# Kernel tuning notes

Measured on AMD Instinct MI355X. Metric: run time of the kernel, lower is better.

The kernel has to match this reference:

```python
import jax, jax.numpy as jnp
import numpy as np

B, IN, H, L, OUT, T, S0 = 512, 64, 512, 2, 12, 31, 8
HEAD = (T - 1) / 2  # 15.0
EPS = 1e-5


def setup_inputs() -> dict:
    key = jax.random.key(0)
    ks = jax.random.split(key, 10)
    s = 0.05
    return {
        "Wih0": jax.random.normal(ks[0], (4 * H, IN), jnp.float32) * s,
        "Whh0": jax.random.normal(ks[1], (4 * H, H), jnp.float32) * s,
        "b0": jax.random.normal(ks[2], (4 * H,), jnp.float32) * s,
        "Wih1": jax.random.normal(ks[3], (4 * H, H), jnp.float32) * s,
        "Whh1": jax.random.normal(ks[4], (4 * H, H), jnp.float32) * s,
        "b1": jax.random.normal(ks[5], (4 * H,), jnp.float32) * s,
        "gamma": jnp.ones((H,), jnp.float32),
        "beta": jnp.zeros((H,), jnp.float32),
        "Wout": jax.random.normal(ks[6], (OUT, H), jnp.float32) * s,
        "bout": jax.random.normal(ks[7], (OUT,), jnp.float32) * s,
        "h0": jax.random.uniform(ks[8], (L, H), jnp.float32),
        "c0": jax.random.uniform(ks[9], (L, H), jnp.float32),
    }


def _lstm_layer(xs, h0, c0, Wih, Whh, b):
    # xs: (B, d_in) treated as an unbatched sequence of length B (torch semantics here).
    def step(carry, x):
        h, c = carry
        g = x @ Wih.T + h @ Whh.T + b  # (4H,)
        i, f, gg, o = jnp.split(g, 4, axis=-1)  # torch gate order: i, f, g, o
        c = jax.nn.sigmoid(f) * c + jax.nn.sigmoid(i) * jnp.tanh(gg)
        h = jax.nn.sigmoid(o) * jnp.tanh(c)
        return (h, c), h
    (hT, cT), ys = jax.lax.scan(step, (h0, c0), xs)
    return ys, hT, cT


def reference(Wih0, Whh0, b0, Wih1, Whh1, b1, gamma, beta, Wout, bout, h0, c0):
    keys = jax.random.split(jax.random.key(42), T)
    x = jnp.ones((B, IN), jnp.float32)
    h, c = h0, c0  # (L, H)
    acts, lps = [], []
    for i in range(T):
        ys0, h0n, c0n = _lstm_layer(x, h[0], c[0], Wih0, Whh0, b0)
        ys1, h1n, c1n = _lstm_layer(ys0, h[1], c[1], Wih1, Whh1, b1)
        h = jnp.stack([h0n, h1n])
        c = jnp.stack([c0n, c1n])
        # BatchNorm1d, training mode (biased variance over the B dim)
        mu = ys1.mean(0)
        var = ys1.var(0)
        yn = (ys1 - mu) / jnp.sqrt(var + EPS) * gamma + beta
        g = jnp.exp(-yn ** 2)  # GaussianActivation
        logits = g @ Wout.T + bout  # (B, OUT)
        if i < HEAD:
            action = jax.random.categorical(keys[i], logits, axis=-1)
        else:
            action = jax.random.categorical(keys[i], logits[:, S0:], axis=-1) + S0
        # log_prob under the FULL categorical (as in the original code)
        lp = jax.nn.log_softmax(logits, axis=-1)[jnp.arange(B), action]
        acts.append(action)
        lps.append(lp)
    return jnp.stack(acts), jnp.stack(lps)  # ((T,B) int, (T,B) float)
```

## Files before the change

### kernel.cpp

```cpp
#include <hip/hip_runtime.h>
#include <stdint.h>
#include <math.h>

#define Bv      512
#define INv     64
#define Hv      512
#define OUTv    12
#define Tv      31
#define S0v     8
#define STEPS   (Tv*Bv)

#define KA      16
#define KB      32
#define KPP     16
#define NBLK    (KA+KB+KPP)
#define RING    32


__device__ __forceinline__ uint32_t rotl32(uint32_t v, int r){ return (v<<r)|(v>>(32-r)); }

__device__ __forceinline__ void threefry2x32(uint32_t k0, uint32_t k1,
                                             uint32_t x0, uint32_t x1,
                                             uint32_t& o0, uint32_t& o1) {
  uint32_t ks2 = k0 ^ k1 ^ 0x1BD11BDAu;
  x0 += k0; x1 += k1;
#define TFR(r) { x0 += x1; x1 = rotl32(x1, r); x1 ^= x0; }
  TFR(13) TFR(15) TFR(26) TFR(6)
  x0 += k1;  x1 += ks2 + 1u;
  TFR(17) TFR(29) TFR(16) TFR(24)
  x0 += ks2; x1 += k0 + 2u;
  TFR(13) TFR(15) TFR(26) TFR(6)
  x0 += k0;  x1 += k1 + 3u;
  TFR(17) TFR(29) TFR(16) TFR(24)
  x0 += k1;  x1 += ks2 + 4u;
  TFR(13) TFR(15) TFR(26) TFR(6)
  x0 += ks2; x1 += k0 + 5u;
#undef TFR
  o0 = x0; o1 = x1;
}

__device__ __forceinline__ uint32_t tf_bits32(uint32_t k0, uint32_t k1, uint32_t j) {
  uint32_t a, b;
  threefry2x32(k0, k1, 0u, j, a, b);
  return a ^ b;
}

__device__ __forceinline__ float u32_to_uniform(uint32_t bits) {
  float f = __uint_as_float(0x3F800000u | (bits >> 9)) - 1.0f;
  const float TINY = 1.17549435e-38f;
  return fmaxf(TINY, f + TINY);
}

__device__ __forceinline__ float gumbelf(uint32_t bits) {
  float u = u32_to_uniform(bits);
  return -logf(-logf(u));
}

__device__ __forceinline__ float sigmf(float x) {
  if (x >= 0.f) { float z = expf(-x); return 1.f/(1.f+z); }
  float z = expf(x); return z/(1.f+z);
}

template<int N>
__device__ __forceinline__ void bfly_halve(float* v, int m) {
  int lane = threadIdx.x & 63;
  bool up = (lane & m) != 0;
#pragma unroll
  for (int j = 0; j < N/2; ++j) {
    float send = up ? v[j] : v[j + N/2];
    float recv = __shfl_xor(send, m, 64);
    v[j] = (up ? v[j + N/2] : v[j]) + recv;
  }
}

__device__ __forceinline__ uint64_t aload64(const uint64_t* p){
  return __hip_atomic_load(p, __ATOMIC_RELAXED, __HIP_MEMORY_SCOPE_AGENT);
}
__device__ __forceinline__ void astore64(uint64_t* p, uint64_t v){
  __hip_atomic_store(p, v, __ATOMIC_RELAXED, __HIP_MEMORY_SCOPE_AGENT);
}
__device__ __forceinline__ uint32_t aload32(const uint32_t* p){
  return __hip_atomic_load(p, __ATOMIC_RELAXED, __HIP_MEMORY_SCOPE_AGENT);
}
__device__ __forceinline__ void astore32(uint32_t* p, uint32_t v){
  __hip_atomic_store(p, v, __ATOMIC_RELAXED, __HIP_MEMORY_SCOPE_AGENT);
}
__device__ __forceinline__ uint32_t tagof(uint64_t w){ return (uint32_t)(w>>32); }
__device__ __forceinline__ float    valof(uint64_t w){ return __uint_as_float((uint32_t)w); }
__device__ __forceinline__ uint64_t mkword(uint32_t t, float v){
  return ((uint64_t)t<<32) | (uint64_t)__float_as_uint(v);
}

__global__ __launch_bounds__(512, 1)
void net_persistent(const float* __restrict__ Wih0, const float* __restrict__ Whh0,
                    const float* __restrict__ b0,
                    const float* __restrict__ Wih1, const float* __restrict__ Whh1,
                    const float* __restrict__ b1,
                    const float* __restrict__ gamma, const float* __restrict__ beta,
                    const float* __restrict__ Wout, const float* __restrict__ bout,
                    const float* __restrict__ h0in, const float* __restrict__ c0in,
                    float* __restrict__ out, uint32_t* __restrict__ wsu)
{
  uint32_t* iterflag = wsu;
  uint64_t* h0A = (uint64_t*)((char*)wsu + 4096);
  uint64_t* h0B = (uint64_t*)((char*)wsu + 4096 + (size_t)RING*Hv*8);
  uint64_t* y1c = (uint64_t*)((char*)wsu + 4096 + (size_t)2*RING*Hv*8);
  float*    ys1 = (float*)((char*)wsu + 4096 + (size_t)3*RING*Hv*8);

  const int bid  = blockIdx.x;
  const int tid  = threadIdx.x;
  const int wave = tid >> 6;
  const int lane = tid & 63;

  __shared__ float hbuf[2][Hv];
  __shared__ float xbuf[2][2*Hv];
  __shared__ float Wout_s[OUTv*Hv];
  __shared__ float mu_s[Hv], isd_s[Hv], gam_s[Hv], bet_s[Hv];

  if (bid < KA) {
    const int hbase = bid*32;
    float w[128];
#pragma unroll
    for (int jl = 0; jl < 4; ++jl)
#pragma unroll
      for (int g = 0; g < 4; ++g) {
        int r = jl*4 + g;
        const float* rp = Whh0 + (size_t)(g*Hv + hbase + wave*4 + jl)*Hv;
#pragma unroll
        for (int k = 0; k < 2; ++k) {
          float4 q = *(const float4*)(rp + k*256 + lane*4);
          w[r*8+k*4+0]=q.x; w[r*8+k*4+1]=q.y; w[r*8+k*4+2]=q.z; w[r*8+k*4+3]=q.w;
        }
      }
    const int jsel = lane & 3;
    const int hg = hbase + wave*4 + jsel;
    float cgi, cgf, cgg, cgo;
    {
      float s0=b0[0*Hv+hg], s1=b0[1*Hv+hg], s2=b0[2*Hv+hg], s3=b0[3*Hv+hg];
      for (int k = 0; k < INv; ++k) {
        s0 += Wih0[(size_t)(0*Hv+hg)*INv+k];
        s1 += Wih0[(size_t)(1*Hv+hg)*INv+k];
        s2 += Wih0[(size_t)(2*Hv+hg)*INv+k];
        s3 += Wih0[(size_t)(3*Hv+hg)*INv+k];
      }
      cgi=s0; cgf=s1; cgg=s2; cgo=s3;
    }
    float cst = c0in[hg];

    for (int s = 0; s < STEPS; ++s) {
      const int par = s & 1;
      if ((s & 15) == 0 && s >= 32) {
        const uint64_t* tp = y1c + (size_t)((s-17)&(RING-1))*Hv + lane*8;
        uint32_t need = (uint32_t)(s - 16);
        for (;;) {
          uint32_t t = tagof(aload64(tp));
          if (__all((int)(t >= need && t <= (uint32_t)STEPS))) break;
          __builtin_amdgcn_s_sleep(1);
        }
      }
      {
        int idx = tid;
        if (s == 0) {
          hbuf[0][idx] = h0in[idx];
        } else {
          const uint64_t* src = h0A + (size_t)((s-1)&(RING-1))*Hv + idx;
          uint32_t want = (uint32_t)s;
          uint64_t a = aload64(src);
          while (tagof(a) != want) a = aload64(src);
          hbuf[par][idx] = valof(a);
        }
      }
      __syncthreads();
      const float4* hv = (const float4*)(hbuf[par]);
      float4 vA = hv[lane], vB = hv[64 + lane];
      float acc[16];
#pragma unroll
      for (int r = 0; r < 16; ++r) {
        float a = 0.f;
        a = fmaf(w[r*8+0], vA.x, a); a = fmaf(w[r*8+1], vA.y, a);
        a = fmaf(w[r*8+2], vA.z, a); a = fmaf(w[r*8+3], vA.w, a);
        a = fmaf(w[r*8+4], vB.x, a); a = fmaf(w[r*8+5], vB.y, a);
        a = fmaf(w[r*8+6], vB.z, a); a = fmaf(w[r*8+7], vB.w, a);
        acc[r] = a;
      }
      bfly_halve<16>(acc, 32);
      bfly_halve<8>(acc, 16);
      bfly_halve<4>(acc, 8);
      bfly_halve<2>(acc, 4);
      acc[0] += __shfl_xor(acc[0], 2, 64);
      acc[0] += __shfl_xor(acc[0], 1, 64);
      float gi = __shfl(acc[0], 16*jsel + 0,  64);
      float gf = __shfl(acc[0], 16*jsel + 4,  64);
      float gg = __shfl(acc[0], 16*jsel + 8,  64);
      float go = __shfl(acc[0], 16*jsel + 12, 64);
      float cc = sigmf(gf+cgf)*cst + sigmf(gi+cgi)*tanhf(gg+cgg);
      float hh = sigmf(go+cgo)*tanhf(cc);
      cst = cc;
      if (lane < 8) {
        uint64_t* dst = (lane < 4) ? h0A : h0B;
        astore64(dst + (size_t)(s&(RING-1))*Hv + hg, mkword((uint32_t)(s+1), hh));
      }
    }
  } else if (bid < KA + KB) {
    const int wg1 = bid - KA;
    const int hbase = wg1*16;
    float w[128];
#pragma unroll
    for (int jl = 0; jl < 2; ++jl)
#pragma unroll
      for (int g = 0; g < 4; ++g) {
        int r = jl*4 + g;
        int row = g*Hv + hbase + wave*2 + jl;
#pragma unroll
        for (int k = 0; k < 4; ++k) {
          int col = k*256 + lane*4;
          const float* M = (col < Hv) ? (Wih1 + (size_t)row*Hv + col)
                                      : (Whh1 + (size_t)row*Hv + (col - Hv));
          float4 q = *(const float4*)M;
          w[r*16+k*4+0]=q.x; w[r*16+k*4+1]=q.y; w[r*16+k*4+2]=q.z; w[r*16+k*4+3]=q.w;
        }
      }
    const int jsel = lane & 1;
    const int hg = hbase + wave*2 + jsel;
    float cgi = b1[0*Hv+hg], cgf = b1[1*Hv+hg],
          cgg = b1[2*Hv+hg], cgo = b1[3*Hv+hg];
    float cst = c0in[Hv + hg];

    for (int s = 0; s < STEPS; ++s) {
      const int par = s & 1;
      {
        int j0 = tid*2;
        if (j0 < Hv) {
          const uint64_t* src = h0B + (size_t)(s&(RING-1))*Hv + j0;
          uint32_t want = (uint32_t)(s+1);
          uint64_t a = aload64(src), b2 = aload64(src+1);
          while (tagof(a) != want || tagof(b2) != want) {
            a = aload64(src); b2 = aload64(src+1);
          }
          xbuf[par][j0] = valof(a); xbuf[par][j0+1] = valof(b2);
        } else {
          if (s == 0) {
            xbuf[0][j0]   = h0in[j0];
            xbuf[0][j0+1] = h0in[j0+1];
          } else {
            const uint64_t* src = y1c + (size_t)((s-1)&(RING-1))*Hv + (j0 - Hv);
            uint32_t want = (uint32_t)s;
            uint64_t a = aload64(src), b2 = aload64(src+1);
            while (tagof(a) != want || tagof(b2) != want) {
              a = aload64(src); b2 = aload64(src+1);
            }
            xbuf[par][j0] = valof(a); xbuf[par][j0+1] = valof(b2);
          }
        }
      }
      __syncthreads();
      const float4* xv = (const float4*)(xbuf[par]);
      float4 v0 = xv[lane], v1 = xv[64+lane], v2 = xv[128+lane], v3 = xv[192+lane];
      float acc[8];
#pragma unroll
      for (int r = 0; r < 8; ++r) {
        float a = 0.f;
        a = fmaf(w[r*16+ 0], v0.x, a); a = fmaf(w[r*16+ 1], v0.y, a);
        a = fmaf(w[r*16+ 2], v0.z, a); a = fmaf(w[r*16+ 3], v0.w, a);
        a = fmaf(w[r*16+ 4], v1.x, a); a = fmaf(w[r*16+ 5], v1.y, a);
        a = fmaf(w[r*16+ 6], v1.z, a); a = fmaf(w[r*16+ 7], v1.w, a);
        a = fmaf(w[r*16+ 8], v2.x, a); a = fmaf(w[r*16+ 9], v2.y, a);
        a = fmaf(w[r*16+10], v2.z, a); a = fmaf(w[r*16+11], v2.w, a);
        a = fmaf(w[r*16+12], v3.x, a); a = fmaf(w[r*16+13], v3.y, a);
        a = fmaf(w[r*16+14], v3.z, a); a = fmaf(w[r*16+15], v3.w, a);
        acc[r] = a;
      }
      bfly_halve<8>(acc, 32);
      bfly_halve<4>(acc, 16);
      bfly_halve<2>(acc, 8);
      acc[0] += __shfl_xor(acc[0], 4, 64);
      acc[0] += __shfl_xor(acc[0], 2, 64);
      acc[0] += __shfl_xor(acc[0], 1, 64);
      float gi = __shfl(acc[0], 32*jsel + 0,  64);
      float gf = __shfl(acc[0], 32*jsel + 8,  64);
      float gg = __shfl(acc[0], 32*jsel + 16, 64);
      float go = __shfl(acc[0], 32*jsel + 24, 64);
      float cc = sigmf(gf+cgf)*cst + sigmf(gi+cgi)*tanhf(gg+cgg);
      float hh = sigmf(go+cgo)*tanhf(cc);
      cst = cc;
      if (lane < 2) {
        astore64(y1c + (size_t)(s&(RING-1))*Hv + hg, mkword((uint32_t)(s+1), hh));
        ys1[(size_t)s*Hv + hg] = hh;
      }
      if ((s & 511) == 511) {
        __syncthreads();
        if (tid == 0) {
          __builtin_amdgcn_fence(__ATOMIC_RELEASE, "agent");
          astore32(iterflag + wg1, (uint32_t)((s >> 9) + 1));
        }
      }
    }
  } else {
    const int p = bid - KA - KB;
    for (int r = tid; r < OUTv*Hv; r += 512) Wout_s[r] = Wout[r];
    for (int h = tid; h < Hv; h += 512) { gam_s[h] = gamma[h]; bet_s[h] = beta[h]; }
    float bo[OUTv];
#pragma unroll
    for (int o = 0; o < OUTv; ++o) bo[o] = bout[o];
    __syncthreads();

    for (int i = p; i < Tv; i += KPP) {
      const uint32_t tgt = (uint32_t)(i + 1);
      if (tid < 64) {
        for (;;) {
          uint32_t v = aload32(iterflag + (lane & 31));
          if (__all((int)(v >= tgt && v <= (uint32_t)Tv))) break;
          __builtin_amdgcn_s_sleep(16);
        }
      }
      __syncthreads();
      __builtin_amdgcn_fence(__ATOMIC_ACQUIRE, "agent");

      const float* Y = ys1 + (size_t)i * Bv * Hv;

      for (int h = tid; h < Hv; h += 512) {
        double sum = 0.0, sq = 0.0;
        for (int b = 0; b < Bv; ++b) {
          double v = (double)Y[(size_t)b*Hv + h];
          sum += v; sq += v*v;
        }
        double mu = sum * (1.0/512.0);
        double var = sq * (1.0/512.0) - mu*mu;
        if (var < 0.0) var = 0.0;
        mu_s[h]  = (float)mu;
        isd_s[h] = (float)(1.0 / sqrt(var + 1e-5));
      }
      __syncthreads();

      uint32_t k0, k1;
      threefry2x32(0u, 42u, 0u, (uint32_t)i, k0, k1);

      for (int b = tid; b < Bv; b += 512) {
        float lg[OUTv];
#pragma unroll
        for (int o = 0; o < OUTv; ++o) lg[o] = 0.f;
        const float* Yb = Y + (size_t)b * Hv;
        for (int h = 0; h < Hv; ++h) {
          float yn = (Yb[h] - mu_s[h]) * isd_s[h] * gam_s[h] + bet_s[h];
          float gv = expf(-yn*yn);
#pragma unroll
          for (int o = 0; o < OUTv; ++o) lg[o] = fmaf(gv, Wout_s[o*Hv + h], lg[o]);
        }
#pragma unroll
        for (int o = 0; o < OUTv; ++o) lg[o] += bo[o];

        int action; float la;
        if (i < 15) {
          float best = -3.0e38f; int bi = 0; float bl = lg[0];
#pragma unroll
          for (int o = 0; o < OUTv; ++o) {
            uint32_t bits = tf_bits32(k0, k1, (uint32_t)(b*12 + o));
            float z = gumbelf(bits) + lg[o];
            if (z > best) { best = z; bi = o; bl = lg[o]; }
          }
          action = bi; la = bl;
        } else {
          float best = -3.0e38f; int bi = 0; float bl = lg[S0v];
#pragma unroll
          for (int o = 0; o < 4; ++o) {
            uint32_t bits = tf_bits32(k0, k1, (uint32_t)(b*4 + o));
            float z = gumbelf(bits) + lg[S0v + o];
            if (z > best) { best = z; bi = o; bl = lg[S0v + o]; }
          }
          action = S0v + bi; la = bl;
        }

        float mx = lg[0];
#pragma unroll
        for (int o = 1; o < OUTv; ++o) mx = fmaxf(mx, lg[o]);
        float se = 0.f;
#pragma unroll
        for (int o = 0; o < OUTv; ++o) se += expf(lg[o] - mx);
        float lp = (la - mx) - logf(se);

        out[i*Bv + b]         = (float)action;
        out[STEPS + i*Bv + b] = lp;
      }
    }
  }
}

extern "C" void kernel_launch(void* const* d_in, const int* in_sizes, int n_in,
                              void* d_out, int out_size, void* d_ws, size_t ws_size,
                              hipStream_t stream) {
  const float* Wih0 = (const float*)d_in[0];
  const float* Whh0 = (const float*)d_in[1];
  const float* b0   = (const float*)d_in[2];
  const float* Wih1 = (const float*)d_in[3];
  const float* Whh1 = (const float*)d_in[4];
  const float* b1   = (const float*)d_in[5];
  const float* gam  = (const float*)d_in[6];
  const float* bet  = (const float*)d_in[7];
  const float* Wout = (const float*)d_in[8];
  const float* bout = (const float*)d_in[9];
  const float* h0   = (const float*)d_in[10];
  const float* c0   = (const float*)d_in[11];

  net_persistent<<<dim3(NBLK), dim3(512), 0, stream>>>(
      Wih0, Whh0, b0, Wih1, Whh1, b1, gam, bet, Wout, bout, h0, c0,
      (float*)d_out, (uint32_t*)d_ws);
}
```

Measured before the change: 41.22 ms.

## Double block size to 1024 threads and halve recurrent LSTM block counts

Blocks now run 1024 threads, and the layer-0 and layer-1 LSTM groups use half as many blocks, each owning twice as many hidden units. Fewer blocks have to poll the cross-block tag handshakes each timestep, and layer-1 input gathering moves to one element per thread. Per-block __syncthreads now spans 16 waves, and the 128-register weight arrays under launch_bounds(1024) may push register pressure to the limit or cause spills. The iterflag poll is adjusted to 16 layer-1 blocks.

After: 134.0 ms. +225.1%, slower.

```diff
diff --git a/kernel.cpp b/kernel.cpp
--- a/kernel.cpp
+++ b/kernel.cpp
@@ -10,8 +10,8 @@
 #define S0v     8
 #define STEPS   (Tv*Bv)
 
-#define KA      16
-#define KB      32
+#define KA      8
+#define KB      16
 #define KPP     16
 #define NBLK    (KA+KB+KPP)
 #define RING    32
@@ -91,7 +91,7 @@
   return ((uint64_t)t<<32) | (uint64_t)__float_as_uint(v);
 }
 
-__global__ __launch_bounds__(512, 1)
+__global__ __launch_bounds__(1024, 1)
 void net_persistent(const float* __restrict__ Wih0, const float* __restrict__ Whh0,
                     const float* __restrict__ b0,
                     const float* __restrict__ Wih1, const float* __restrict__ Whh1,
@@ -118,7 +118,7 @@
   __shared__ float mu_s[Hv], isd_s[Hv], gam_s[Hv], bet_s[Hv];
 
   if (bid < KA) {
-    const int hbase = bid*32;
+    const int hbase = bid*64;
     float w[128];
 #pragma unroll
     for (int jl = 0; jl < 4; ++jl)
@@ -158,16 +158,15 @@
           __builtin_amdgcn_s_sleep(1);
         }
       }
-      {
-        int idx = tid;
+      if (tid < Hv) {
         if (s == 0) {
-          hbuf[0][idx] = h0in[idx];
+          hbuf[0][tid] = h0in[tid];
         } else {
-          const uint64_t* src = h0A + (size_t)((s-1)&(RING-1))*Hv + idx;
+          const uint64_t* src = h0A + (size_t)((s-1)&(RING-1))*Hv + tid;
           uint32_t want = (uint32_t)s;
           uint64_t a = aload64(src);
           while (tagof(a) != want) a = aload64(src);
-          hbuf[par][idx] = valof(a);
+          hbuf[par][tid] = valof(a);
         }
       }
       __syncthreads();
@@ -203,7 +202,7 @@
     }
   } else if (bid < KA + KB) {
     const int wg1 = bid - KA;
-    const int hbase = wg1*16;
+    const int hbase = wg1*32;
     float w[128];
 #pragma unroll
     for (int jl = 0; jl < 2; ++jl)
@@ -228,29 +227,21 @@
 
     for (int s = 0; s < STEPS; ++s) {
       const int par = s & 1;
-      {
-        int j0 = tid*2;
-        if (j0 < Hv) {
-          const uint64_t* src = h0B + (size_t)(s&(RING-1))*Hv + j0;
-          uint32_t want = (uint32_t)(s+1);
-          uint64_t a = aload64(src), b2 = aload64(src+1);
-          while (tagof(a) != want || tagof(b2) != want) {
-            a = aload64(src); b2 = aload64(src+1);
-          }
-          xbuf[par][j0] = valof(a); xbuf[par][j0+1] = valof(b2);
+      if (tid < Hv) {
+        const uint64_t* src = h0B + (size_t)(s&(RING-1))*Hv + tid;
+        uint32_t want = (uint32_t)(s+1);
+        uint64_t a = aload64(src);
+        while (tagof(a) != want) a = aload64(src);
+        xbuf[par][tid] = valof(a);
+      } else {
+        if (s == 0) {
+          xbuf[0][tid] = h0in[tid];
         } else {
-          if (s == 0) {
-            xbuf[0][j0]   = h0in[j0];
-            xbuf[0][j0+1] = h0in[j0+1];
-          } else {
-            const uint64_t* src = y1c + (size_t)((s-1)&(RING-1))*Hv + (j0 - Hv);
-            uint32_t want = (uint32_t)s;
-            uint64_t a = aload64(src), b2 = aload64(src+1);
-            while (tagof(a) != want || tagof(b2) != want) {
-              a = aload64(src); b2 = aload64(src+1);
-            }
-            xbuf[par][j0] = valof(a); xbuf[par][j0+1] = valof(b2);
-          }
+          const uint64_t* src = y1c + (size_t)((s-1)&(RING-1))*Hv + (tid - Hv);
+          uint32_t want = (uint32_t)s;
+          uint64_t a = aload64(src);
+          while (tagof(a) != want) a = aload64(src);
+          xbuf[par][tid] = valof(a);
         }
       }
       __syncthreads();
@@ -297,8 +288,8 @@
     }
   } else {
     const int p = bid - KA - KB;
-    for (int r = tid; r < OUTv*Hv; r += 512) Wout_s[r] = Wout[r];
-    for (int h = tid; h < Hv; h += 512) { gam_s[h] = gamma[h]; bet_s[h] = beta[h]; }
+    for (int r = tid; r < OUTv*Hv; r += 1024) Wout_s[r] = Wout[r];
+    for (int h = tid; h < Hv; h += 1024) { gam_s[h] = gamma[h]; bet_s[h] = beta[h]; }
     float bo[OUTv];
 #pragma unroll
     for (int o = 0; o < OUTv; ++o) bo[o] = bout[o];
@@ -308,7 +299,7 @@
       const uint32_t tgt = (uint32_t)(i + 1);
       if (tid < 64) {
         for (;;) {
-          uint32_t v = aload32(iterflag + (lane & 31));
+          uint32_t v = aload32(iterflag + (lane & 15));
           if (__all((int)(v >= tgt && v <= (uint32_t)Tv))) break;
           __builtin_amdgcn_s_sleep(16);
         }
@@ -318,7 +309,7 @@
 
       const float* Y = ys1 + (size_t)i * Bv * Hv;
 
-      for (int h = tid; h < Hv; h += 512) {
+      for (int h = tid; h < Hv; h += 1024) {
         double sum = 0.0, sq = 0.0;
         for (int b = 0; b < Bv; ++b) {
           double v = (double)Y[(size_t)b*Hv + h];
@@ -335,7 +326,7 @@
       uint32_t k0, k1;
       threefry2x32(0u, 42u, 0u, (uint32_t)i, k0, k1);
 
-      for (int b = tid; b < Bv; b += 512) {
+      for (int b = tid; b < Bv; b += 1024) {
         float lg[OUTv];
 #pragma unroll
         for (int o = 0; o < OUTv; ++o) lg[o] = 0.f;
@@ -401,7 +392,7 @@
   const float* h0   = (const float*)d_in[10];
   const float* c0   = (const float*)d_in[11];
 
-  net_persistent<<<dim3(NBLK), dim3(512), 0, stream>>>(
+  net_persistent<<<dim3(NBLK), dim3(1024), 0, stream>>>(
       Wih0, Whh0, b0, Wih1, Whh1, b1, gam, bet, Wout, bout, h0, c0,
       (float*)d_out, (uint32_t*)d_ws);
 }
```
